# Kernel tuning notes

Measured on AMD Instinct MI355X. Metric: run time of the kernel, lower is better.

Reference implementation:

```python
import jax, jax.numpy as jnp
import numpy as np
import math

B, S, D, H = 2, 2048, 512, 8  # batch, seq, d_hidden (= per-head dim here), n_heads


def _rope(x):
    # x: [B, H, S, D]; standard interleaved RoPE with base 10000
    b, h, s, d = x.shape
    inv_freq = 1.0 / (10000.0 ** (jnp.arange(0, d, 2, dtype=jnp.float32) / d))  # [d/2]
    ang = jnp.arange(s, dtype=jnp.float32)[:, None] * inv_freq[None, :]          # [S, d/2]
    cos, sin = jnp.cos(ang), jnp.sin(ang)
    x1, x2 = x[..., 0::2], x[..., 1::2]
    r1 = x1 * cos - x2 * sin
    r2 = x1 * sin + x2 * cos
    return jnp.stack([r1, r2], axis=-1).reshape(b, h, s, d).astype(x.dtype)


def setup_inputs() -> dict:
    key = jax.random.key(0)
    kq, k1, k2, k3, k4 = jax.random.split(key, 5)
    std = 0.02
    return {
        "q": jax.random.normal(kq, (B, S, D), dtype=jnp.float32),
        "W_q": jax.random.normal(k1, (H, D, D), dtype=jnp.float32) * std,
        "W_k": jax.random.normal(k2, (H, D, D), dtype=jnp.float32) * std,
        "W_v": jax.random.normal(k3, (H, D, D), dtype=jnp.float32) * std,
        "W_o": jax.random.normal(k4, (H * D, D), dtype=jnp.float32) * std,
    }


def reference(q, W_q, W_k, W_v, W_o):
    b, s, d = q.shape
    h = W_q.shape[0]
    scale = 1.0 / math.sqrt(d)
    qh = jnp.einsum('bsz,hzd->bhsd', q, W_q)
    kh = jnp.einsum('bsz,hzd->bhsd', q, W_k)
    vh = jnp.einsum('bsz,hzd->bhsd', q, W_v)
    qh = _rope(qh)
    kh = _rope(kh)
    scores = jnp.einsum('bhqd,bhkd->bhqk', qh, kh) * scale
    causal = jnp.triu(jnp.ones((s, s), dtype=bool), k=1)  # True above diagonal
    scores = jnp.where(causal, -jnp.inf, scores)
    probs = jax.nn.softmax(scores, axis=-1)  # dropout is identity in eval
    # NOTE: faithful to the original (transposed) einsum: contracts over the
    # query index z of probs with the sequence index z of v.
    out = jnp.einsum('bhzs,bhzd->bhsd', probs, vh)
    out = out.transpose(0, 2, 1, 3).reshape(b, s, h * d)
    return jnp.einsum('bsz,zd->bsd', out, W_o)
```

## Files before the change

kernel.cpp:

```cpp
#include <hip/hip_runtime.h>
#include <hip/hip_bf16.h>
#include <math.h>
#include <stdint.h>

#define BB 2
#define SS 2048
#define DD 512
#define HH 8
#define NTOK (BB*SS)
#define NQKV (3*HH*DD)
#define BHD  (HH*DD)
#define NBH  (BB*HH)
#define NTILE 136

typedef __attribute__((ext_vector_type(8))) short short8v;
typedef __attribute__((ext_vector_type(4))) float floatx4;

__device__ __forceinline__ unsigned short f2bf(float f) {
  unsigned int u = __builtin_bit_cast(unsigned int, f);
  u = (u + 0x7FFFu + ((u >> 16) & 1u)) >> 16;
  return (unsigned short)u;
}
__device__ __forceinline__ float bf2f(unsigned short s) {
  unsigned int u = ((unsigned int)s) << 16;
  return __builtin_bit_cast(float, u);
}
__device__ __forceinline__ void async16(const void* g, void* l) {
  __builtin_amdgcn_global_load_lds(
      (const __attribute__((address_space(1))) unsigned int*)g,
      (__attribute__((address_space(3))) unsigned int*)l, 16, 0, 0);
}

__global__ void k_convert_q(const float* __restrict__ q, unsigned short* __restrict__ qbf) {
  int i = (blockIdx.x * 256 + threadIdx.x) * 4;
  const float4 v = *(const float4*)&q[i];
  ushort4 o;
  o.x = f2bf(v.x); o.y = f2bf(v.y); o.z = f2bf(v.z); o.w = f2bf(v.w);
  *(ushort4*)&qbf[i] = o;
}

__global__ void k_rope_tab(float* __restrict__ rope) {
  const int idx = blockIdx.x * 256 + threadIdx.x;
  const int s = idx >> 8, dp = idx & 255;
  const float inv = exp2f(-13.287712379549449f * (1.0f/256.0f) * (float)dp);
  float sn, cs;
  __sincosf((float)s * inv, &sn, &cs);
  rope[(size_t)idx * 2]     = cs;
  rope[(size_t)idx * 2 + 1] = sn;
}

__global__ void k_prep_w(const float* __restrict__ Wq, const float* __restrict__ Wk,
                         const float* __restrict__ Wv, const float* __restrict__ Wo,
                         unsigned short* __restrict__ Wcat, unsigned short* __restrict__ Wot) {
  __shared__ float t[32][33];
  const int z = blockIdx.z;
  const float* in; unsigned short* out; int inLD, outLD;
  float sc = 1.0f;
  if (z < 24) {
    int tsel = z / 8, h = z % 8;
    const float* w = (tsel == 0) ? Wq : (tsel == 1) ? Wk : Wv;
    if (tsel == 0) sc = 0.044194173824159216f;
    in = w + (size_t)h * DD * DD;
    out = Wcat + ((size_t)tsel * BHD + (size_t)h * DD) * DD;
    inLD = DD; outLD = DD;
  } else {
    int k = z - 24;
    in = Wo + (size_t)k * DD * DD;
    out = Wot + (size_t)k * DD;
    inLD = DD; outLD = BHD;
  }
  const int tx = threadIdx.x, ty = threadIdx.y;
  const int bx = blockIdx.x * 32, by = blockIdx.y * 32;
  for (int kk = 0; kk < 4; ++kk)
    t[ty + 8*kk][tx] = in[(size_t)(by + ty + 8*kk) * inLD + bx + tx];
  __syncthreads();
  for (int kk = 0; kk < 4; ++kk)
    out[(size_t)(bx + ty + 8*kk) * outLD + by + tx] = f2bf(t[tx][ty + 8*kk] * sc);
}

__global__ __launch_bounds__(256, 2)
void k_qkv(const unsigned short* __restrict__ Abf, const unsigned short* __restrict__ Bt,
           const float* __restrict__ ropeT,
           unsigned short* __restrict__ Qr, unsigned short* __restrict__ Kr,
           unsigned short* __restrict__ Vt) {
  __shared__ short As[2][128*32];
  __shared__ short Bs[2][256*32];
  const int tid = threadIdx.x;
  const int m0 = blockIdx.x * 128;
  const int n0 = blockIdx.y * 256;
  const int wave = tid >> 6, lane = tid & 63, qd = lane >> 4, c = lane & 15;
  const int wm = (wave >> 1) * 64, wn = (wave & 1) * 128;
  floatx4 acc[4][8] = {};
  const int e0 = tid * 8;
  const int r0 = e0 >> 5, c0 = e0 & 31;
  auto STAGE = [&](int buf, int k0) {
    async16(&Abf[(size_t)(m0 + r0      ) * 512 + k0 + c0], &As[buf][e0]);
    async16(&Abf[(size_t)(m0 + r0 +  64) * 512 + k0 + c0], &As[buf][e0 + 2048]);
    async16(&Bt [(size_t)(n0 + r0      ) * 512 + k0 + c0], &Bs[buf][e0]);
    async16(&Bt [(size_t)(n0 + r0 +  64) * 512 + k0 + c0], &Bs[buf][e0 + 2048]);
    async16(&Bt [(size_t)(n0 + r0 + 128) * 512 + k0 + c0], &Bs[buf][e0 + 4096]);
    async16(&Bt [(size_t)(n0 + r0 + 192) * 512 + k0 + c0], &Bs[buf][e0 + 6144]);
  };
  STAGE(0, 0);
  __syncthreads();
  for (int k0 = 0; k0 < 512; k0 += 32) {
    const int cur = (k0 >> 5) & 1;
    if (k0 < 480) STAGE(cur ^ 1, k0 + 32);
    short8v a[4], bfr[8];
    for (int mt = 0; mt < 4; ++mt) a[mt]   = *(const short8v*)&As[cur][(wm + mt*16 + c)*32 + qd*8];
    for (int nt = 0; nt < 8; ++nt) bfr[nt] = *(const short8v*)&Bs[cur][(wn + nt*16 + c)*32 + qd*8];
    for (int mt = 0; mt < 4; ++mt)
      for (int nt = 0; nt < 8; ++nt)
        acc[mt][nt] = __builtin_amdgcn_mfma_f32_16x16x32_bf16(a[mt], bfr[nt], acc[mt][nt], 0, 0, 0);
    __syncthreads();
  }
  const int tsel = n0 >> 12;
  const int h = (n0 >> 9) & 7;
  const int bat = m0 >> 11;
  const int bh = bat * HH + h;
  const int dloc = (n0 & 511) + wn;
  if (tsel < 2) {
    unsigned short* dst = (tsel == 0) ? Qr : Kr;
    const int dp0 = (dloc >> 1) + (c >> 1);
    const unsigned int sgn = (c & 1) ? 0u : 0x80000000u;
    for (int mt = 0; mt < 4; ++mt) {
      const int mrow = (m0 & 2047) + wm + mt*16 + qd*4;
      for (int r = 0; r < 4; ++r) {
        const int s = mrow + r;
        const float2* rp = (const float2*)&ropeT[((size_t)s * 256 + dp0) * 2];
        const size_t ob = ((size_t)bh * SS + s) * DD;
        for (int nt = 0; nt < 8; ++nt) {
          const float2 tt = rp[nt * 8];
          const float v = acc[mt][nt][r];
          float p = __shfl_xor(v, 1, 64);
          p = __builtin_bit_cast(float, __builtin_bit_cast(unsigned int, p) ^ sgn);
          dst[ob + dloc + nt*16 + c] = f2bf(fmaf(p, tt.y, v * tt.x));
        }
      }
    }
  } else {
    for (int nt = 0; nt < 8; ++nt) {
      const int d = dloc + nt*16 + c;
      const size_t vbase = ((size_t)bh * DD + d) * SS;
      for (int mt = 0; mt < 4; ++mt) {
        const int s = (m0 & 2047) + wm + mt*16 + qd*4;
        ushort4 u;
        u.x = f2bf(acc[mt][nt][0]); u.y = f2bf(acc[mt][nt][1]);
        u.z = f2bf(acc[mt][nt][2]); u.w = f2bf(acc[mt][nt][3]);
        *(ushort4*)&Vt[vbase + s] = u;
      }
    }
  }
}

__global__ __launch_bounds__(256)
void k_scores(const unsigned short* __restrict__ Qr, const unsigned short* __restrict__ Kr,
              unsigned short* __restrict__ Eg, float* __restrict__ lsum) {
  __shared__ short UN[17408];
  unsigned short* ET = (unsigned short*)UN;
  const int tid = threadIdx.x;
  const int bh = blockIdx.y;
  const int t = blockIdx.x;
  int zb = 0;
  while (((zb + 1) * (zb + 2)) / 2 <= t) ++zb;
  const int st = t - (zb * (zb + 1)) / 2;
  const int z0 = zb * 128, s0 = st * 128;
  const int wave = tid >> 6, lane = tid & 63, qd = lane >> 4, c = lane & 15;
  const int wm = (wave >> 1) * 64, wn = (wave & 1) * 64;
  const size_t qb = (size_t)bh * SS * DD;
  floatx4 acc[4][4] = {};
  const int e0 = tid * 8, e1 = e0 + 2048;
  const int r0 = e0 >> 5, c0 = e0 & 31, r1 = e1 >> 5, c1 = e1 & 31;
  auto STAGE = [&](int buf, int k0) {
    short* A = UN + buf * 4096;
    short* B = UN + 8192 + buf * 4096;
    async16(&Qr[qb + (size_t)(z0 + r0) * 512 + k0 + c0], &A[e0]);
    async16(&Qr[qb + (size_t)(z0 + r1) * 512 + k0 + c1], &A[e1]);
    async16(&Kr[qb + (size_t)(s0 + r0) * 512 + k0 + c0], &B[e0]);
    async16(&Kr[qb + (size_t)(s0 + r1) * 512 + k0 + c1], &B[e1]);
  };
  STAGE(0, 0);
  __syncthreads();
  for (int kk = 0; kk < 16; ++kk) {
    const int cur = kk & 1;
    if (kk < 15) STAGE(cur ^ 1, (kk + 1) * 32);
    const short* Asp = UN + cur * 4096;
    const short* Bsp = UN + 8192 + cur * 4096;
    short8v a[4], bfr[4];
    for (int mt = 0; mt < 4; ++mt) a[mt]   = *(const short8v*)&Asp[(wm + mt*16 + c)*32 + qd*8];
    for (int nt = 0; nt < 4; ++nt) bfr[nt] = *(const short8v*)&Bsp[(wn + nt*16 + c)*32 + qd*8];
    for (int mt = 0; mt < 4; ++mt)
      for (int nt = 0; nt < 4; ++nt)
        acc[mt][nt] = __builtin_amdgcn_mfma_f32_16x16x32_bf16(a[mt], bfr[nt], acc[mt][nt], 0, 0, 0);
    __syncthreads();
  }
  const bool diag = (st == zb);
  for (int mt = 0; mt < 4; ++mt) {
    const int zl = wm + mt*16 + qd*4;
    float rs[4] = {0.f, 0.f, 0.f, 0.f};
    for (int nt = 0; nt < 4; ++nt) {
      const int sl = wn + nt*16 + c;
      for (int r = 0; r < 4; ++r) {
        float ev = __expf(acc[mt][nt][r]);
        if (diag && (sl > zl + r)) ev = 0.f;
        acc[mt][nt][r] = ev;
        rs[r] += ev;
      }
    }
    for (int off = 1; off < 16; off <<= 1)
      for (int r = 0; r < 4; ++r) rs[r] += __shfl_xor(rs[r], off, 64);
    if (c == 0)
      for (int r = 0; r < 4; ++r)
        atomicAdd(&lsum[(size_t)bh * SS + z0 + zl + r], rs[r]);
  }
  for (int mt = 0; mt < 4; ++mt) {
    const int zl = wm + mt*16 + qd*4;
    for (int nt = 0; nt < 4; ++nt) {
      const int sl = wn + nt*16 + c;
      ushort4 u;
      u.x = f2bf(acc[mt][nt][0]); u.y = f2bf(acc[mt][nt][1]);
      u.z = f2bf(acc[mt][nt][2]); u.w = f2bf(acc[mt][nt][3]);
      *(ushort4*)&ET[sl * 136 + zl] = u;
    }
  }
  __syncthreads();
  const size_t tb = ((size_t)bh * NTILE + t) * 16384;
  for (int it = 0; it < 8; ++it) {
    const int e = it * 2048 + tid * 8;
    const int row = e >> 7, col = e & 127;
    *(short8v*)&Eg[tb + row * 128 + col] = *(const short8v*)&ET[row * 136 + col];
  }
}

__global__ void k_vscale(unsigned short* __restrict__ Vt, const float* __restrict__ lsum) {
  const int idx = (blockIdx.x * 256 + threadIdx.x) * 8;
  const int z = idx & (SS - 1);
  const int bh = idx >> 20;
  short8v v = *(const short8v*)&Vt[idx];
  const float* lp = &lsum[(size_t)bh * SS + z];
  short8v o;
  for (int i = 0; i < 8; ++i)
    o[i] = (short)f2bf(bf2f((unsigned short)v[i]) / lp[i]);
  *(short8v*)&Vt[idx] = o;
}

__global__ __launch_bounds__(256)
void k_pv(const unsigned short* __restrict__ Eg, const unsigned short* __restrict__ Vs,
          unsigned short* __restrict__ Ocat) {
  __shared__ short Vl[2][2][128*32];
  __shared__ short El[2][2][128*32];
  const int tid = threadIdx.x;
  const int d0 = blockIdx.x * 128;
  const int pr = blockIdx.y;
  const int bh = blockIdx.z;
  const int bat = bh >> 3, h = bh & 7;
  const int wave = tid >> 6, lane = tid & 63, qd = lane >> 4, c = lane & 15;
  const int wm = (wave >> 1) * 64, wn = (wave & 1) * 64;
  const size_t vbb = (size_t)bh * DD * SS;
  const int e = tid * 8;
  auto STAGE = [&](int buf, int zb, int half, int st) {
    const size_t tb = ((size_t)bh * NTILE + (zb * (zb + 1)) / 2 + st) * 16384;
    const int zbase = zb * 128 + half * 64;
    for (int i = 0; i < 4; ++i) {
      const int ee = e + i * 2048;
      const int kc = ee >> 12, row = (ee >> 5) & 127, col = ee & 31;
      async16(&Vs[vbb + (size_t)(d0 + row) * SS + zbase + kc * 32 + col], &Vl[buf][kc][row * 32 + col]);
    }
    for (int i = 0; i < 4; ++i) {
      const int ee = e + i * 2048;
      const int kc = ee >> 12, row = (ee >> 5) & 127, col = ee & 31;
      async16(&Eg[tb + (size_t)row * 128 + half * 64 + kc * 32 + col], &El[buf][kc][row * 32 + col]);
    }
  };
  for (int sel = 0; sel < 2; ++sel) {
    const int st = sel ? (15 - pr) : pr;
    const int s0 = st * 128;
    floatx4 acc[4][4] = {};
    const int nst = (16 - st) * 2;
    STAGE(0, st, 0, st);
    __syncthreads();
    for (int q2 = 0; q2 < nst; ++q2) {
      const int cur = q2 & 1;
      if (q2 + 1 < nst) STAGE(cur ^ 1, st + ((q2 + 1) >> 1), (q2 + 1) & 1, st);
      for (int kc = 0; kc < 2; ++kc) {
        short8v a[4], b[4];
        for (int dt = 0; dt < 4; ++dt) a[dt] = *(const short8v*)&Vl[cur][kc][(wm + dt*16 + c)*32 + qd*8];
        for (int nt = 0; nt < 4; ++nt) b[nt] = *(const short8v*)&El[cur][kc][(wn + nt*16 + c)*32 + qd*8];
        for (int dt = 0; dt < 4; ++dt)
          for (int nt = 0; nt < 4; ++nt)
            acc[dt][nt] = __builtin_amdgcn_mfma_f32_16x16x32_bf16(a[dt], b[nt], acc[dt][nt], 0, 0, 0);
      }
      __syncthreads();
    }
    for (int nt = 0; nt < 4; ++nt) {
      const int sg = s0 + wn + nt*16 + c;
      const size_t ob = ((size_t)(bat * SS + sg)) * BHD + (size_t)h * DD + d0;
      for (int dt = 0; dt < 4; ++dt) {
        const int dloc = wm + dt*16 + qd*4;
        ushort4 u;
        u.x = f2bf(acc[dt][nt][0]); u.y = f2bf(acc[dt][nt][1]);
        u.z = f2bf(acc[dt][nt][2]); u.w = f2bf(acc[dt][nt][3]);
        *(ushort4*)&Ocat[ob + dloc] = u;
      }
    }
  }
}

__global__ __launch_bounds__(256)
void k_oproj(const unsigned short* __restrict__ Ocat, const unsigned short* __restrict__ Wot,
             float* __restrict__ out) {
  __shared__ short As[2][2][128*32];
  __shared__ short Bs[2][2][128*32];
  const int tid = threadIdx.x;
  const int m0 = blockIdx.x * 128;
  const int n0 = blockIdx.y * 128;
  const int ks = blockIdx.z * 1024;
  const int wave = tid >> 6, lane = tid & 63, qd = lane >> 4, c = lane & 15;
  const int wm = (wave >> 1) * 64, wn = (wave & 1) * 64;
  floatx4 acc[4][4] = {};
  const int e0 = tid * 8, e1 = e0 + 2048;
  const int r0 = e0 >> 5, c0 = e0 & 31, r1 = e1 >> 5, c1 = e1 & 31;
  auto STAGE = [&](int buf, int k0) {
    for (int kc = 0; kc < 2; ++kc) {
      const int kk = k0 + kc * 32;
      async16(&Ocat[(size_t)(m0 + r0) * BHD + kk + c0], &As[buf][kc][e0]);
      async16(&Ocat[(size_t)(m0 + r1) * BHD + kk + c1], &As[buf][kc][e1]);
      async16(&Wot [(size_t)(n0 + r0) * BHD + kk + c0], &Bs[buf][kc][e0]);
      async16(&Wot [(size_t)(n0 + r1) * BHD + kk + c1], &Bs[buf][kc][e1]);
    }
  };
  STAGE(0, ks);
  __syncthreads();
  for (int t = 0; t < 16; ++t) {
    const int cur = t & 1;
    if (t < 15) STAGE(cur ^ 1, ks + (t + 1) * 64);
    for (int kc = 0; kc < 2; ++kc) {
      short8v a[4], b[4];
      for (int mt = 0; mt < 4; ++mt) a[mt] = *(const short8v*)&As[cur][kc][(wm + mt*16 + c)*32 + qd*8];
      for (int nt = 0; nt < 4; ++nt) b[nt] = *(const short8v*)&Bs[cur][kc][(wn + nt*16 + c)*32 + qd*8];
      for (int mt = 0; mt < 4; ++mt)
        for (int nt = 0; nt < 4; ++nt)
          acc[mt][nt] = __builtin_amdgcn_mfma_f32_16x16x32_bf16(a[mt], b[nt], acc[mt][nt], 0, 0, 0);
    }
    __syncthreads();
  }
  for (int mt = 0; mt < 4; ++mt) {
    const int m = m0 + wm + mt*16 + qd*4;
    for (int nt = 0; nt < 4; ++nt) {
      const int n = n0 + wn + nt*16 + c;
      for (int r = 0; r < 4; ++r)
        atomicAdd(&out[(size_t)(m + r) * DD + n], acc[mt][nt][r]);
    }
  }
}

extern "C" void kernel_launch(void* const* d_in, const int* in_sizes, int n_in,
                              void* d_out, int out_size, void* d_ws, size_t ws_size,
                              hipStream_t stream) {
  const float* q  = (const float*)d_in[0];
  const float* Wq = (const float*)d_in[1];
  const float* Wk = (const float*)d_in[2];
  const float* Wv = (const float*)d_in[3];
  const float* Wo = (const float*)d_in[4];

  char* base = (char*)d_ws;
  unsigned short* Eg   = (unsigned short*)base;
  unsigned short* qbf  = (unsigned short*)base;
  unsigned short* Wcat = (unsigned short*)(base + 4194304);
  float*          rope = (float*)(base + 16777216);
  char* p = base + 71303168;
  unsigned short* Wot  = (unsigned short*)p; p += 4194304;
  unsigned short* Qr   = (unsigned short*)p;
  unsigned short* Ocat = (unsigned short*)p; p += 33554432;
  unsigned short* Kr   = (unsigned short*)p; p += 33554432;
  unsigned short* Vt   = (unsigned short*)p; p += 33554432;
  float*          lsum = (float*)p;

  hipMemsetAsync(lsum, 0, (size_t)NBH * SS * 4, stream);
  hipMemsetAsync(d_out, 0, (size_t)NTOK * DD * 4, stream);

  k_convert_q<<<NTOK*DD/1024, 256, 0, stream>>>(q, qbf);
  k_rope_tab<<<SS*256/256, 256, 0, stream>>>(rope);
  k_prep_w<<<dim3(16,16,32), dim3(32,8), 0, stream>>>(Wq, Wk, Wv, Wo, Wcat, Wot);
  k_qkv<<<dim3(32,48), 256, 0, stream>>>(qbf, Wcat, rope, Qr, Kr, Vt);
  k_scores<<<dim3(NTILE,16), 256, 0, stream>>>(Qr, Kr, Eg, lsum);
  k_vscale<<<NBH*DD*SS/(256*8), 256, 0, stream>>>(Vt, lsum);
  k_pv<<<dim3(4,8,16), 256, 0, stream>>>(Eg, Vt, Ocat);
  k_oproj<<<dim3(32,4,4), 256, 0, stream>>>(Ocat, Wot, (float*)d_out);
}
```

Before: 407.3 us.

## Use partial vmcnt waits and XCD-aware block remapping in GEMM kernels

Replaces __syncthreads (which waits for all outstanding async global-to-LDS loads) with an explicit s_waitcnt vmcnt(N) plus a raw barrier. The current buffer's loads complete while the prefetch of the next buffer stays in flight during the MFMA work. Also remaps linear block IDs so that consecutive blocks dispatched round-robin across the 8 XCDs share data within each XCD's L2. This relies on the compiler not reordering the async loads and on the vmcnt counts exactly matching the issued loads. A wrong count would cause a data race.

New measurement: 373.7 us. 1.09x faster.

```diff
diff --git a/kernel.cpp b/kernel.cpp
--- a/kernel.cpp
+++ b/kernel.cpp
@@ -30,6 +30,8 @@
       (const __attribute__((address_space(1))) unsigned int*)g,
       (__attribute__((address_space(3))) unsigned int*)l, 16, 0, 0);
 }
+#define WAITVM(N) asm volatile("s_waitcnt vmcnt(" #N ")" ::: "memory")
+#define BAR() __builtin_amdgcn_s_barrier()
 
 __global__ void k_convert_q(const float* __restrict__ q, unsigned short* __restrict__ qbf) {
   int i = (blockIdx.x * 256 + threadIdx.x) * 4;
@@ -86,8 +88,10 @@
   __shared__ short As[2][128*32];
   __shared__ short Bs[2][256*32];
   const int tid = threadIdx.x;
-  const int m0 = blockIdx.x * 128;
-  const int n0 = blockIdx.y * 256;
+  const int lin = blockIdx.y * 32 + blockIdx.x;
+  const int lin2 = (lin & 7) * 192 + (lin >> 3);
+  const int m0 = (lin2 & 31) * 128;
+  const int n0 = (lin2 >> 5) * 256;
   const int wave = tid >> 6, lane = tid & 63, qd = lane >> 4, c = lane & 15;
   const int wm = (wave >> 1) * 64, wn = (wave & 1) * 128;
   floatx4 acc[4][8] = {};
@@ -102,17 +106,18 @@
     async16(&Bt [(size_t)(n0 + r0 + 192) * 512 + k0 + c0], &Bs[buf][e0 + 6144]);
   };
   STAGE(0, 0);
-  __syncthreads();
   for (int k0 = 0; k0 < 512; k0 += 32) {
     const int cur = (k0 >> 5) & 1;
-    if (k0 < 480) STAGE(cur ^ 1, k0 + 32);
+    if (k0 < 480) { STAGE(cur ^ 1, k0 + 32); WAITVM(6); }
+    else          { WAITVM(0); }
+    BAR();
     short8v a[4], bfr[8];
     for (int mt = 0; mt < 4; ++mt) a[mt]   = *(const short8v*)&As[cur][(wm + mt*16 + c)*32 + qd*8];
     for (int nt = 0; nt < 8; ++nt) bfr[nt] = *(const short8v*)&Bs[cur][(wn + nt*16 + c)*32 + qd*8];
     for (int mt = 0; mt < 4; ++mt)
       for (int nt = 0; nt < 8; ++nt)
         acc[mt][nt] = __builtin_amdgcn_mfma_f32_16x16x32_bf16(a[mt], bfr[nt], acc[mt][nt], 0, 0, 0);
-    __syncthreads();
+    BAR();
   }
   const int tsel = n0 >> 12;
   const int h = (n0 >> 9) & 7;
@@ -159,8 +164,10 @@
   __shared__ short UN[17408];
   unsigned short* ET = (unsigned short*)UN;
   const int tid = threadIdx.x;
-  const int bh = blockIdx.y;
-  const int t = blockIdx.x;
+  const int lin = blockIdx.y * 136 + blockIdx.x;
+  const int lin2 = (lin & 7) * 272 + (lin >> 3);
+  const int bh = lin2 / 136;
+  const int t = lin2 % 136;
   int zb = 0;
   while (((zb + 1) * (zb + 2)) / 2 <= t) ++zb;
   const int st = t - (zb * (zb + 1)) / 2;
@@ -180,10 +187,11 @@
     async16(&Kr[qb + (size_t)(s0 + r1) * 512 + k0 + c1], &B[e1]);
   };
   STAGE(0, 0);
-  __syncthreads();
   for (int kk = 0; kk < 16; ++kk) {
     const int cur = kk & 1;
-    if (kk < 15) STAGE(cur ^ 1, (kk + 1) * 32);
+    if (kk < 15) { STAGE(cur ^ 1, (kk + 1) * 32); WAITVM(4); }
+    else         { WAITVM(0); }
+    BAR();
     const short* Asp = UN + cur * 4096;
     const short* Bsp = UN + 8192 + cur * 4096;
     short8v a[4], bfr[4];
@@ -192,7 +200,7 @@
     for (int mt = 0; mt < 4; ++mt)
       for (int nt = 0; nt < 4; ++nt)
         acc[mt][nt] = __builtin_amdgcn_mfma_f32_16x16x32_bf16(a[mt], bfr[nt], acc[mt][nt], 0, 0, 0);
-    __syncthreads();
+    BAR();
   }
   const bool diag = (st == zb);
   for (int mt = 0; mt < 4; ++mt) {
@@ -250,9 +258,11 @@
   __shared__ short Vl[2][2][128*32];
   __shared__ short El[2][2][128*32];
   const int tid = threadIdx.x;
-  const int d0 = blockIdx.x * 128;
-  const int pr = blockIdx.y;
-  const int bh = blockIdx.z;
+  const int lin = (blockIdx.z * 8 + blockIdx.y) * 4 + blockIdx.x;
+  const int lin2 = (lin & 7) * 64 + (lin >> 3);
+  const int d0 = (lin2 & 3) * 128;
+  const int pr = (lin2 >> 2) & 7;
+  const int bh = lin2 >> 5;
   const int bat = bh >> 3, h = bh & 7;
   const int wave = tid >> 6, lane = tid & 63, qd = lane >> 4, c = lane & 15;
   const int wm = (wave >> 1) * 64, wn = (wave & 1) * 64;
@@ -278,10 +288,11 @@
     floatx4 acc[4][4] = {};
     const int nst = (16 - st) * 2;
     STAGE(0, st, 0, st);
-    __syncthreads();
     for (int q2 = 0; q2 < nst; ++q2) {
       const int cur = q2 & 1;
-      if (q2 + 1 < nst) STAGE(cur ^ 1, st + ((q2 + 1) >> 1), (q2 + 1) & 1, st);
+      if (q2 + 1 < nst) { STAGE(cur ^ 1, st + ((q2 + 1) >> 1), (q2 + 1) & 1, st); WAITVM(8); }
+      else              { WAITVM(0); }
+      BAR();
       for (int kc = 0; kc < 2; ++kc) {
         short8v a[4], b[4];
         for (int dt = 0; dt < 4; ++dt) a[dt] = *(const short8v*)&Vl[cur][kc][(wm + dt*16 + c)*32 + qd*8];
@@ -290,7 +301,7 @@
           for (int nt = 0; nt < 4; ++nt)
             acc[dt][nt] = __builtin_amdgcn_mfma_f32_16x16x32_bf16(a[dt], b[nt], acc[dt][nt], 0, 0, 0);
       }
-      __syncthreads();
+      BAR();
     }
     for (int nt = 0; nt < 4; ++nt) {
       const int sg = s0 + wn + nt*16 + c;
@@ -312,9 +323,12 @@
   __shared__ short As[2][2][128*32];
   __shared__ short Bs[2][2][128*32];
   const int tid = threadIdx.x;
-  const int m0 = blockIdx.x * 128;
-  const int n0 = blockIdx.y * 128;
-  const int ks = blockIdx.z * 1024;
+  const int lin = (blockIdx.z * 4 + blockIdx.y) * 32 + blockIdx.x;
+  const int lin2 = (lin & 7) * 64 + (lin >> 3);
+  const int m0 = (lin2 & 31) * 128;
+  const int rest = lin2 >> 5;
+  const int n0 = (rest & 3) * 128;
+  const int ks = (rest >> 2) * 1024;
   const int wave = tid >> 6, lane = tid & 63, qd = lane >> 4, c = lane & 15;
   const int wm = (wave >> 1) * 64, wn = (wave & 1) * 64;
   floatx4 acc[4][4] = {};
@@ -330,10 +344,11 @@
     }
   };
   STAGE(0, ks);
-  __syncthreads();
   for (int t = 0; t < 16; ++t) {
     const int cur = t & 1;
-    if (t < 15) STAGE(cur ^ 1, ks + (t + 1) * 64);
+    if (t < 15) { STAGE(cur ^ 1, ks + (t + 1) * 64); WAITVM(8); }
+    else        { WAITVM(0); }
+    BAR();
     for (int kc = 0; kc < 2; ++kc) {
       short8v a[4], b[4];
       for (int mt = 0; mt < 4; ++mt) a[mt] = *(const short8v*)&As[cur][kc][(wm + mt*16 + c)*32 + qd*8];
@@ -342,7 +357,7 @@
         for (int nt = 0; nt < 4; ++nt)
           acc[mt][nt] = __builtin_amdgcn_mfma_f32_16x16x32_bf16(a[mt], b[nt], acc[mt][nt], 0, 0, 0);
     }
-    __syncthreads();
+    BAR();
   }
   for (int mt = 0; mt < 4; ++mt) {
     const int m = m0 + wm + mt*16 + qd*4;
```
